# Kernel tuning notes

Measured on AMD Instinct MI355X. Metric: run time of the kernel, lower is better.

## Reference

```python
import jax, jax.numpy as jnp
import numpy as np

N_HEADS = 8
N_POINTS = 4
LN_EPS = 1e-5


def _ln(x, g, b):
    m = jnp.mean(x, -1, keepdims=True)
    v = jnp.mean((x - m) ** 2, -1, keepdims=True)
    return (x - m) * jax.lax.rsqrt(v + LN_EPS) * g + b


def _mha(q, k, v, wq, bq, wk, bk, wv, bv, wo, bo):
    B, Lq, C = q.shape
    Dh = C // N_HEADS
    Q = (q @ wq.T + bq).reshape(B, Lq, N_HEADS, Dh)
    K = (k @ wk.T + bk).reshape(B, -1, N_HEADS, Dh)
    V = (v @ wv.T + bv).reshape(B, -1, N_HEADS, Dh)
    s = jnp.einsum('bqhd,bkhd->bhqk', Q, K) * (1.0 / float(np.sqrt(Dh)))
    a = jax.nn.softmax(s, -1)
    o = jnp.einsum('bhqk,bkhd->bqhd', a, V).reshape(B, Lq, C)
    return o @ wo.T + bo


def _ref_points(h, w, L):
    ry = jnp.linspace(0.5, h - 0.5, h) / h
    rx = jnp.linspace(0.5, w - 0.5, w) / w
    gy, gx = jnp.meshgrid(ry, rx, indexing='ij')
    ref = jnp.stack([gx.reshape(-1), gy.reshape(-1)], -1)[None]  # (1, h*w, 2)
    return jnp.broadcast_to(ref[:, :, None, :], (1, h * w, L, 2))


def _deform_core(value, shapes, starts, loc, aw):
    # value: (B, Len_in, H, Dh); loc: (B, Lq, H, L, P, 2); aw: (B, Lq, H, L, P)
    B, _, H, Dh = value.shape
    Lq, P = loc.shape[1], loc.shape[4]
    out = jnp.zeros((B, H, Lq, Dh), value.dtype)
    for l in range(shapes.shape[0]):
        Hl, Wl = int(shapes[l, 0]), int(shapes[l, 1])
        s = int(starts[l])
        v = value[:, s:s + Hl * Wl].transpose(0, 2, 1, 3)  # (B, H, Hl*Wl, Dh)
        # grid_sample(align_corners=False, padding_mode='zeros') pixel coords
        xl = loc[:, :, :, l, :, 0] * Wl - 0.5  # (B, Lq, H, P)
        yl = loc[:, :, :, l, :, 1] * Hl - 0.5
        x0 = jnp.floor(xl); y0 = jnp.floor(yl)
        fx = xl - x0; fy = yl - y0
        x0 = x0.astype(jnp.int32); y0 = y0.astype(jnp.int32)
        acc = jnp.zeros((B, H, Lq, P, Dh), value.dtype)
        for dy, dx in ((0, 0), (0, 1), (1, 0), (1, 1)):
            xi = x0 + dx; yi = y0 + dy
            wgt = (fx if dx else 1.0 - fx) * (fy if dy else 1.0 - fy)
            valid = ((xi >= 0) & (xi < Wl) & (yi >= 0) & (yi < Hl)).astype(value.dtype)
            idx = (jnp.clip(yi, 0, Hl - 1) * Wl + jnp.clip(xi, 0, Wl - 1))
            idx = idx.transpose(0, 2, 1, 3).reshape(B, H, Lq * P)
            g = jnp.take_along_axis(v, idx[..., None], axis=2).reshape(B, H, Lq, P, Dh)
            acc = acc + g * (wgt * valid).transpose(0, 2, 1, 3)[..., None]
        out = out + jnp.einsum('bhqpd,bqhp->bhqd', acc, aw[:, :, :, l])
    return out.transpose(0, 2, 1, 3).reshape(B, Lq, H * Dh)


def reference(tgt, query_pos, src, wq, bq, wk, bk, wv, bv, wo, bo, ln2_g, ln2_b,
              w_off, b_off, w_attn, b_attn, w_val, b_val, w_cout, b_cout,
              ln1_g, ln1_b, w1, b1, w2, b2, ln3_g, ln3_b,
              src_spatial_shapes, level_start_index, h, w):
    shapes = np.asarray(src_spatial_shapes)
    starts = np.asarray(level_start_index)
    h = int(h); w = int(w)
    L = shapes.shape[0]
    B, Lq, C = tgt.shape
    Dh = C // N_HEADS
    # --- self attention (post-LN residual) ---
    q = tgt + query_pos
    t2 = _mha(q, q, tgt, wq, bq, wk, bk, wv, bv, wo, bo)
    t = _ln(tgt + t2, ln2_g, ln2_b)
    # --- MSDeformAttn cross attention ---
    qc = t + query_pos
    value = (src @ w_val.T + b_val).reshape(B, -1, N_HEADS, Dh)
    off = (qc @ w_off.T + b_off).reshape(B, Lq, N_HEADS, L, N_POINTS, 2)
    aw = (qc @ w_attn.T + b_attn).reshape(B, Lq, N_HEADS, L * N_POINTS)
    aw = jax.nn.softmax(aw, -1).reshape(B, Lq, N_HEADS, L, N_POINTS)
    norm = jnp.stack([shapes[:, 1].astype(np.float32), shapes[:, 0].astype(np.float32)], -1)  # (L,2): (W,H)
    rp = _ref_points(h, w, L)  # (1, Lq, L, 2)
    loc = rp[:, :, None, :, None, :] + off / norm[None, None, None, :, None, :]
    samp = _deform_core(value, shapes, starts, loc, aw)
    t2 = samp @ w_cout.T + b_cout
    t = _ln(t + t2, ln1_g, ln1_b)
    # --- FFN ---
    t2 = jax.nn.relu(t @ w1.T + b1) @ w2.T + b2
    t = _ln(t + t2, ln3_g, ln3_b)
    return t


def setup_inputs() -> dict:
    key = jax.random.key(0)
    B, C, L, P, dff = 2, 256, 4, 4, 1024
    h = w = 48
    shapes = np.array([[48, 48], [24, 24], [12, 12], [6, 6]], np.int32)
    starts = np.array([0, 2304, 2880, 3024], np.int32)
    Len_in = 3060
    Lq = h * w
    ks = iter(jax.random.split(key, 40))
    def rn(shape, s=0.02):
        return jax.random.normal(next(ks), shape, jnp.float32) * s
    return dict(
        tgt=rn((B, Lq, C), 1.0), query_pos=rn((B, Lq, C), 1.0), src=rn((B, Len_in, C), 1.0),
        wq=rn((C, C)), bq=rn((C,)), wk=rn((C, C)), bk=rn((C,)), wv=rn((C, C)), bv=rn((C,)),
        wo=rn((C, C)), bo=rn((C,)),
        ln2_g=jnp.ones((C,)), ln2_b=jnp.zeros((C,)),
        w_off=rn((N_HEADS * L * P * 2, C)), b_off=rn((N_HEADS * L * P * 2,)),
        w_attn=rn((N_HEADS * L * P, C)), b_attn=rn((N_HEADS * L * P,)),
        w_val=rn((C, C)), b_val=rn((C,)), w_cout=rn((C, C)), b_cout=rn((C,)),
        ln1_g=jnp.ones((C,)), ln1_b=jnp.zeros((C,)),
        w1=rn((dff, C)), b1=rn((dff,)), w2=rn((C, dff)), b2=rn((C,)),
        ln3_g=jnp.ones((C,)), ln3_b=jnp.zeros((C,)),
        src_spatial_shapes=shapes, level_start_index=starts, h=h, w=w)
```

## Files before the change

kernel.cpp:

```cpp
#include <hip/hip_runtime.h>
#include <hip/hip_bf16.h>
#include <math.h>

typedef __hip_bfloat16 bf16;
typedef __attribute__((ext_vector_type(8))) short short8;
typedef __attribute__((ext_vector_type(4))) short short4v;
typedef __attribute__((ext_vector_type(4))) float f32x4;

static constexpr int B   = 2;
static constexpr int LQ  = 2304;
static constexpr int C   = 256;
static constexpr int NH  = 8;
static constexpr int DH  = 32;
static constexpr int NL  = 4;
static constexpr int NP  = 4;
static constexpr int LEN = 3060;
static constexpr int DFF = 1024;
static constexpr int MQ  = B * LQ;
static constexpr int MV  = B * LEN;
static constexpr int SZ1 = MQ * C;

#define MFMA16(a, b, c) __builtin_amdgcn_mfma_f32_16x16x32_bf16(a, b, c, 0, 0, 0)

__device__ __forceinline__ float ldf(const void* p, size_t i, int bf) {
  return bf ? __bfloat162float(((const bf16*)p)[i]) : ((const float*)p)[i];
}
__device__ __forceinline__ short fl2s(float v) {
  bf16 h = __float2bfloat16(v);
  return *(short*)&h;
}
__device__ __forceinline__ short fl2s_fast(float v) {
  union { float f; unsigned u; } x; x.f = v;
  return (short)((x.u + 0x8000u) >> 16);
}
__device__ __forceinline__ float s2fl(short s) {
  return __bfloat162float(*(bf16*)&s);
}
__device__ __forceinline__ int wire_is_bf16(const unsigned* gprobe) {
  return gprobe[0] == 0x3F803F80u;
}
__device__ __forceinline__ float ldbias(const void* b, int n, int fl) {
  return fl ? s2fl(((const short*)b)[n]) : s2fl(fl2s(((const float*)b)[n]));
}
__device__ __forceinline__ short8 add2bf(short8 a, short8 b) {
  short8 r;
#pragma unroll
  for (int j = 0; j < 8; ++j) r[j] = fl2s(s2fl(a[j]) + s2fl(b[j]));
  return r;
}

struct GemmJob {
  int Xmode;
  const short* Xbf; const void* Xwire; const void* Xwire2;
  const void* Wwire; const void* bwire;
  void* Y;
  int M, N, K, ldY, col0, relu, out_mode, nblk_x;
  float qscale;
};
struct GemmBatch { GemmJob j[4]; int start[5]; int njobs; };

template <int MR>
__global__ __launch_bounds__(256) void gemm_mfma(GemmBatch nb,
                                                 const unsigned* __restrict__ gprobe) {
  constexpr int MT = MR / 64;
  const int fl = wire_is_bf16(gprobe);
  int id = blockIdx.x;
  int jj = 0;
  while (jj + 1 < nb.njobs && id >= nb.start[jj + 1]) ++jj;
  const GemmJob jb = nb.j[jj];
  const int local = id - nb.start[jj];
  const int bx = local % jb.nblk_x;
  const int by = local / jb.nblk_x;
  const int M = jb.M, N = jb.N, K = jb.K;

  __shared__ short Xs[MR][72];
  __shared__ short Ws[64][72];
  const int tid = threadIdx.x;
  const int wave = tid >> 6, lane = tid & 63;
  const int quad = lane >> 4, l16 = lane & 15;
  const int m0 = bx * MR, n0 = by * 64;
  f32x4 acc[MT][4];
#pragma unroll
  for (int mt = 0; mt < MT; ++mt)
#pragma unroll
    for (int nt = 0; nt < 4; ++nt) acc[mt][nt] = f32x4{0.f, 0.f, 0.f, 0.f};

  const int xrow = (MR == 128) ? (tid >> 1) : (tid >> 2);
  const int xcol = (MR == 128) ? ((tid & 1) * 32) : ((tid & 3) * 16);
  constexpr int XU = (MR == 128) ? 4 : 2;
  const int wrow = tid >> 2;
  const int wcol = (tid & 3) * 16;
  int xr = m0 + xrow; if (xr >= M) xr = M - 1;

  const short* xp16 = nullptr; const float* xpf = nullptr;
  const short* tp16 = nullptr; const short* pp16 = nullptr;
  const float* tpf  = nullptr; const float* ppf  = nullptr;
  if (jb.Xmode == 0) {
    xp16 = jb.Xbf + (size_t)xr * K;
  } else if (jb.Xmode == 2) {
    if (fl) xp16 = (const short*)jb.Xwire + (size_t)xr * K;
    else    xpf  = (const float*)jb.Xwire + (size_t)xr * K;
  } else {
    if (fl) { tp16 = (const short*)jb.Xwire + (size_t)xr * K;
              pp16 = (const short*)jb.Xwire2 + (size_t)xr * K; }
    else    { tpf  = (const float*)jb.Xwire + (size_t)xr * K;
              ppf  = (const float*)jb.Xwire2 + (size_t)xr * K; }
  }
  const short* wp16 = (const short*)jb.Wwire;
  const float* wpf  = (const float*)jb.Wwire;
  const size_t wro = (size_t)(n0 + wrow) * K;

  for (int k0 = 0; k0 < K; k0 += 64) {
    if (xp16) {
#pragma unroll
      for (int u = 0; u < XU; ++u)
        *(short8*)&Xs[xrow][xcol + u * 8] = *(const short8*)(xp16 + k0 + xcol + u * 8);
    } else if (xpf) {
#pragma unroll
      for (int u = 0; u < XU; ++u) {
        const float* s = xpf + k0 + xcol + u * 8;
        short8 r;
#pragma unroll
        for (int j = 0; j < 8; ++j) r[j] = fl2s(s[j]);
        *(short8*)&Xs[xrow][xcol + u * 8] = r;
      }
    } else if (tp16) {
#pragma unroll
      for (int u = 0; u < XU; ++u) {
        short8 t8 = *(const short8*)(tp16 + k0 + xcol + u * 8);
        short8 p8 = *(const short8*)(pp16 + k0 + xcol + u * 8);
        *(short8*)&Xs[xrow][xcol + u * 8] = add2bf(t8, p8);
      }
    } else {
#pragma unroll
      for (int u = 0; u < XU; ++u) {
        const float* t = tpf + k0 + xcol + u * 8;
        const float* p = ppf + k0 + xcol + u * 8;
        short8 r;
#pragma unroll
        for (int j = 0; j < 8; ++j) r[j] = fl2s(t[j] + p[j]);
        *(short8*)&Xs[xrow][xcol + u * 8] = r;
      }
    }
    if (fl) {
      const short* wp = wp16 + wro + k0 + wcol;
      *(short8*)&Ws[wrow][wcol]     = *(const short8*)(wp);
      *(short8*)&Ws[wrow][wcol + 8] = *(const short8*)(wp + 8);
    } else {
      const float* wp = wpf + wro + k0 + wcol;
      short8 w0, w1;
#pragma unroll
      for (int j = 0; j < 8; ++j) { w0[j] = fl2s(wp[j]); w1[j] = fl2s(wp[8 + j]); }
      *(short8*)&Ws[wrow][wcol]     = w0;
      *(short8*)&Ws[wrow][wcol + 8] = w1;
    }
    __syncthreads();
#pragma unroll
    for (int kc = 0; kc < 2; ++kc) {
#pragma unroll
      for (int mt = 0; mt < MT; ++mt) {
        short8 a = *(const short8*)&Xs[wave * (16 * MT) + mt * 16 + l16][kc * 32 + quad * 8];
#pragma unroll
        for (int nt = 0; nt < 4; ++nt) {
          short8 b = *(const short8*)&Ws[nt * 16 + l16][kc * 32 + quad * 8];
          acc[mt][nt] = MFMA16(a, b, acc[mt][nt]);
        }
      }
    }
    __syncthreads();
  }

  if (jb.out_mode == 2) {
#pragma unroll
    for (int mt = 0; mt < MT; ++mt) {
      const int mbase = m0 + wave * (16 * MT) + mt * 16 + quad * 4;
      const int b = mbase / LQ;
      const int qb_ = mbase - b * LQ;
#pragma unroll
      for (int nt = 0; nt < 4; ++nt) {
        const int n = n0 + nt * 16 + l16;
        const float bv = ldbias(jb.bwire, n, fl);
        short4v v4;
#pragma unroll
        for (int r = 0; r < 4; ++r) v4[r] = fl2s(acc[mt][nt][r] + bv);
        *(short4v*)((short*)jb.Y + (size_t)(b * 256 + n) * LQ + qb_) = v4;
      }
    }
    return;
  }
#pragma unroll
  for (int mt = 0; mt < MT; ++mt)
#pragma unroll
    for (int nt = 0; nt < 4; ++nt) {
      const int n = n0 + nt * 16 + l16;
      const float bv = ldbias(jb.bwire, n, fl);
#pragma unroll
      for (int r = 0; r < 4; ++r) {
        const int m = m0 + wave * (16 * MT) + mt * 16 + quad * 4 + r;
        if (m < M) {
          float v = (acc[mt][nt][r] + bv) * jb.qscale;
          if (jb.relu) v = fmaxf(v, 0.f);
          if (jb.out_mode == 1)
            ((short*)jb.Y)[(size_t)m * jb.ldY + jb.col0 + n] = fl2s(v);
          else
            ((float*)jb.Y)[(size_t)m * jb.ldY + jb.col0 + n] = v;
        }
      }
    }
}

__global__ __launch_bounds__(256) void ln_kern(const void* __restrict__ A, int a_mode,
                                               const float* __restrict__ R,
                                               const void* __restrict__ g,
                                               const void* __restrict__ be,
                                               float* __restrict__ Yf32,
                                               short* __restrict__ Y16,
                                               void* __restrict__ Yfinal,
                                               const void* __restrict__ pos,
                                               short* __restrict__ Yqc,
                                               int rows, const unsigned* __restrict__ gprobe) {
  const int fl = wire_is_bf16(gprobe);
  const int row = blockIdx.x * 4 + (threadIdx.x >> 6);
  const int lane = threadIdx.x & 63;
  if (row >= rows) return;
  const int c0 = lane * 4;
  const size_t base = (size_t)row * C + c0;

  float x[4];
  if (a_mode == 1 && fl) {
    short4v a4 = *(const short4v*)((const short*)A + base);
#pragma unroll
    for (int j = 0; j < 4; ++j) x[j] = s2fl(a4[j]);
  } else {
    f32x4 a4 = *(const f32x4*)((const float*)A + base);
#pragma unroll
    for (int j = 0; j < 4; ++j) x[j] = a4[j];
  }
  f32x4 r4 = *(const f32x4*)(R + base);
  float s = 0.f, s2 = 0.f;
#pragma unroll
  for (int j = 0; j < 4; ++j) { x[j] += r4[j]; s += x[j]; s2 += x[j] * x[j]; }
#pragma unroll
  for (int off = 32; off > 0; off >>= 1) {
    s += __shfl_xor(s, off);
    s2 += __shfl_xor(s2, off);
  }
  const float mean = s * (1.f / C);
  const float var = fmaxf(s2 * (1.f / C) - mean * mean, 0.f);
  const float inv = rsqrtf(var + 1e-5f);

  float gv[4], bvv[4];
  if (fl) {
    short4v g4 = *(const short4v*)((const short*)g + c0);
    short4v b4 = *(const short4v*)((const short*)be + c0);
#pragma unroll
    for (int j = 0; j < 4; ++j) { gv[j] = s2fl(g4[j]); bvv[j] = s2fl(b4[j]); }
  } else {
    f32x4 g4 = *(const f32x4*)((const float*)g + c0);
    f32x4 b4 = *(const f32x4*)((const float*)be + c0);
#pragma unroll
    for (int j = 0; j < 4; ++j) { gv[j] = g4[j]; bvv[j] = b4[j]; }
  }
  float y[4];
#pragma unroll
  for (int j = 0; j < 4; ++j) y[j] = (x[j] - mean) * inv * gv[j] + bvv[j];

  if (Yfinal) {
    if (fl) {
      short4v o;
#pragma unroll
      for (int j = 0; j < 4; ++j) o[j] = fl2s(y[j]);
      *(short4v*)((short*)Yfinal + base) = o;
    } else {
      f32x4 o;
#pragma unroll
      for (int j = 0; j < 4; ++j) o[j] = y[j];
      *(f32x4*)((float*)Yfinal + base) = o;
    }
    return;
  }
  if (Yf32) {
    f32x4 o;
#pragma unroll
    for (int j = 0; j < 4; ++j) o[j] = y[j];
    *(f32x4*)(Yf32 + base) = o;
  }
  if (Y16) {
    short4v o;
#pragma unroll
    for (int j = 0; j < 4; ++j) o[j] = fl2s(y[j]);
    *(short4v*)(Y16 + base) = o;
  }
  if (Yqc) {
    float pv[4];
    if (fl) {
      short4v p4 = *(const short4v*)((const short*)pos + base);
#pragma unroll
      for (int j = 0; j < 4; ++j) pv[j] = s2fl(p4[j]);
    } else {
      f32x4 p4 = *(const f32x4*)((const float*)pos + base);
#pragma unroll
      for (int j = 0; j < 4; ++j) pv[j] = p4[j];
    }
    short4v o;
#pragma unroll
    for (int j = 0; j < 4; ++j) o[j] = fl2s(y[j] + pv[j]);
    *(short4v*)(Yqc + base) = o;
  }
}

__global__ __launch_bounds__(256) void flash_attn(const short* __restrict__ QK,
                                                  const short* __restrict__ Vt,
                                                  short* __restrict__ Op) {
  constexpr int LDQK = 512;
  constexpr int NC = LQ / 64;
  constexpr int NQT = 3;
  const int qb = blockIdx.x;
  const int bh = blockIdx.y;
  const int b = bh >> 3, h = bh & 7;
  const int tid = threadIdx.x;
  const int wave = tid >> 6, lane = tid & 63;
  const int quad = lane >> 4, l16 = lane & 15;

  __shared__ short Ps[4][16][68];
  __shared__ float lsh[256];

  const int q0 = qb * 48;
  const size_t rowb = (size_t)(b * LQ);
  const short* kcol = QK + 256 + h * DH + quad * 8;
  const short* vt0 = Vt + (size_t)(b * 256 + h * 32 + l16) * LQ + quad * 8;
  const short* vt1 = Vt + (size_t)(b * 256 + h * 32 + 16 + l16) * LQ + quad * 8;

  short8 qfrag[NQT];
#pragma unroll
  for (int qt = 0; qt < NQT; ++qt)
    qfrag[qt] = *(const short8*)(QK + (rowb + q0 + qt * 16 + l16) * LDQK + h * DH + quad * 8);

  f32x4 o0[NQT], o1[NQT];
  float lrow[NQT];
#pragma unroll
  for (int qt = 0; qt < NQT; ++qt) {
    o0[qt] = f32x4{0.f, 0.f, 0.f, 0.f};
    o1[qt] = f32x4{0.f, 0.f, 0.f, 0.f};
    lrow[qt] = 0.f;
  }

  short8 kf[4], vf[4];
  {
    const int k0 = wave * 64;
#pragma unroll
    for (int kt = 0; kt < 4; ++kt)
      kf[kt] = *(const short8*)(kcol + (rowb + k0 + kt * 16 + l16) * LDQK);
    vf[0] = *(const short8*)(vt0 + k0);
    vf[1] = *(const short8*)(vt0 + k0 + 32);
    vf[2] = *(const short8*)(vt1 + k0);
    vf[3] = *(const short8*)(vt1 + k0 + 32);
  }

  for (int c = wave; c < NC; c += 4) {
    short8 kn[4], vn[4];
    if (c + 4 < NC) {
      const int k0n = (c + 4) * 64;
#pragma unroll
      for (int kt = 0; kt < 4; ++kt)
        kn[kt] = *(const short8*)(kcol + (rowb + k0n + kt * 16 + l16) * LDQK);
      vn[0] = *(const short8*)(vt0 + k0n);
      vn[1] = *(const short8*)(vt0 + k0n + 32);
      vn[2] = *(const short8*)(vt1 + k0n);
      vn[3] = *(const short8*)(vt1 + k0n + 32);
    }

#pragma unroll
    for (int qt = 0; qt < NQT; ++qt) {
      f32x4 s[4];
#pragma unroll
      for (int kt = 0; kt < 4; ++kt) {
        f32x4 z = {0.f, 0.f, 0.f, 0.f};
        s[kt] = MFMA16(kf[kt], qfrag[qt], z);
      }

      float ps = 0.f;
#pragma unroll
      for (int kt = 0; kt < 4; ++kt)
#pragma unroll
        for (int r = 0; r < 4; ++r) {
          float p = __expf(s[kt][r]);
          s[kt][r] = p;
          ps += p;
        }
      lrow[qt] += ps;

#pragma unroll
      for (int kt = 0; kt < 4; ++kt) {
        short4v pk;
#pragma unroll
        for (int r = 0; r < 4; ++r) pk[r] = fl2s_fast(s[kt][r]);
        *(short4v*)&Ps[wave][l16][kt * 16 + quad * 4] = pk;
      }

#pragma unroll
      for (int half = 0; half < 2; ++half) {
        short4v a0 = *(const short4v*)&Ps[wave][l16][half * 32 + quad * 8];
        short4v a1 = *(const short4v*)&Ps[wave][l16][half * 32 + quad * 8 + 4];
        short8 afrag;
#pragma unroll
        for (int j = 0; j < 4; ++j) { afrag[j] = a0[j]; afrag[4 + j] = a1[j]; }
        o0[qt] = MFMA16(afrag, vf[half], o0[qt]);
        o1[qt] = MFMA16(afrag, vf[2 + half], o1[qt]);
      }
    }

#pragma unroll
    for (int kt = 0; kt < 4; ++kt) { kf[kt] = kn[kt]; vf[kt] = vn[kt]; }
  }

  float* obuf = (float*)&Ps[0][0][0];
  for (int qt = 0; qt < NQT; ++qt) {
    __syncthreads();
    lsh[(wave * 4 + quad) * 16 + l16] = lrow[qt];
#pragma unroll
    for (int r = 0; r < 4; ++r) {
      const int q = quad * 4 + r;
      obuf[(wave * 16 + q) * 32 + l16] = o0[qt][r];
      obuf[(wave * 16 + q) * 32 + 16 + l16] = o1[qt][r];
    }
    __syncthreads();
#pragma unroll
    for (int e = tid; e < 512; e += 256) {
      const int q = e >> 5, d = e & 31;
      float lg = 0.f;
#pragma unroll
      for (int i = 0; i < 16; ++i) lg += lsh[i * 16 + q];
      float ov = 0.f;
#pragma unroll
      for (int w = 0; w < 4; ++w) ov += obuf[(w * 16 + q) * 32 + d];
      Op[(rowb + q0 + qt * 16 + q) * C + h * DH + d] = fl2s_fast(ov / lg);
    }
  }
}

__global__ __launch_bounds__(256) void deform_kern(const short* __restrict__ value,
                                                   const float* __restrict__ oa,
                                                   const int* __restrict__ shapes,
                                                   const int* __restrict__ starts,
                                                   const int* __restrict__ hp,
                                                   const int* __restrict__ wp,
                                                   short* __restrict__ samp) {
  const int bq = blockIdx.x * 4 + (threadIdx.x >> 6);
  const int b = bq / LQ, q = bq % LQ;
  const int lane = threadIdx.x & 63;
  const int h_ = lane >> 3;
  const int d0 = (lane & 7) * 4;

  const int w0 = *wp, h0 = *hp;
  const int qx = q % w0, qy = q / w0;
  const float refx = (qx + 0.5f) / (float)w0;
  const float refy = (qy + 0.5f) / (float)h0;

  const float* offp = oa + (size_t)bq * 384 + h_ * 32;
  const float* awraw = oa + (size_t)bq * 384 + 256 + h_ * 16;

  float e[16];
  float mm = -1e30f;
#pragma unroll
  for (int j = 0; j < 16; ++j) mm = fmaxf(mm, awraw[j]);
  float ssum = 0.f;
#pragma unroll
  for (int j = 0; j < 16; ++j) {
    e[j] = __expf(awraw[j] - mm);
    ssum += e[j];
  }
  const float sinv = 1.f / ssum;

  float acc0 = 0.f, acc1 = 0.f, acc2 = 0.f, acc3 = 0.f;
  for (int l = 0; l < NL; ++l) {
    const int Hl = shapes[l * 2 + 0];
    const int Wl = shapes[l * 2 + 1];
    const int st = starts[l];
    const short* vbase = value + ((size_t)(b * LEN + st)) * C + h_ * DH + d0;
#pragma unroll
    for (int p = 0; p < NP; ++p) {
      const float ox = offp[l * 8 + p * 2 + 0];
      const float oy = offp[l * 8 + p * 2 + 1];
      const float a = e[l * 4 + p] * sinv;
      const float xl = refx * Wl + ox - 0.5f;
      const float yl = refy * Hl + oy - 0.5f;
      const float x0f = floorf(xl), y0f = floorf(yl);
      const float fx = xl - x0f, fy = yl - y0f;
      const int x0 = (int)x0f, y0 = (int)y0f;
#pragma unroll
      for (int corner = 0; corner < 4; ++corner) {
        const int dx = corner & 1, dy = corner >> 1;
        const int xi = x0 + dx, yi = y0 + dy;
        const float wx = dx ? fx : 1.f - fx;
        const float wy = dy ? fy : 1.f - fy;
        const bool valid = (xi >= 0) & (xi < Wl) & (yi >= 0) & (yi < Hl);
        if (valid) {
          const float w = a * wx * wy;
          short4v v4 = *(const short4v*)(vbase + (size_t)(yi * Wl + xi) * C);
          acc0 += w * s2fl(v4[0]);
          acc1 += w * s2fl(v4[1]);
          acc2 += w * s2fl(v4[2]);
          acc3 += w * s2fl(v4[3]);
        }
      }
    }
  }
  short4v out;
  out[0] = fl2s(acc0); out[1] = fl2s(acc1); out[2] = fl2s(acc2); out[3] = fl2s(acc3);
  *(short4v*)(samp + (size_t)bq * C + h_ * DH + d0) = out;
}

extern "C" void kernel_launch(void* const* d_in, const int* in_sizes, int n_in,
                              void* d_out, int out_size, void* d_ws, size_t ws_size,
                              hipStream_t stream) {
  const void* tgt       = d_in[0];
  const void* query_pos = d_in[1];
  const void* src       = d_in[2];
  const void* wq = d_in[3];  const void* bq = d_in[4];
  const void* wk = d_in[5];  const void* bk = d_in[6];
  const void* wv = d_in[7];  const void* bv = d_in[8];
  const void* wo = d_in[9];  const void* bo = d_in[10];
  const void* ln2_g = d_in[11]; const void* ln2_b = d_in[12];
  const void* w_off = d_in[13]; const void* b_off = d_in[14];
  const void* w_attn = d_in[15]; const void* b_attn = d_in[16];
  const void* w_val = d_in[17]; const void* b_val = d_in[18];
  const void* w_cout = d_in[19]; const void* b_cout = d_in[20];
  const void* ln1_g = d_in[21]; const void* ln1_b = d_in[22];
  const void* w1 = d_in[23]; const void* b1 = d_in[24];
  const void* w2 = d_in[25]; const void* b2 = d_in[26];
  const void* ln3_g = d_in[27]; const void* ln3_b = d_in[28];
  const int* shapes = (const int*)d_in[29];
  const int* starts = (const int*)d_in[30];
  const int* hp = (const int*)d_in[31];
  const int* wp = (const int*)d_in[32];
  const unsigned* gprobe = (const unsigned*)ln2_g;

  short* q16    = (short*)((char*)d_ws + 256);
  short* qk_out = q16 + SZ1;
  short* vt16   = qk_out + (size_t)MQ * 512;
  short* ao16   = vt16 + SZ1;
  short* valb   = ao16 + SZ1;
  short* ffn1   = valb + (size_t)MV * C;
  short* t1_16  = ffn1 + (size_t)MQ * DFF;
  float* t2a    = (float*)(t1_16 + SZ1);
  float* t_32   = t2a + SZ1;
  float* t1_32  = t_32 + SZ1;
  float* oa     = t1_32 + SZ1;

  const float scale = 1.f / sqrtf((float)DH);
  const dim3 blk(256);
  const int NX128 = MQ / 128;
  const int NX64  = MQ / 64;
  const int NXV   = (MV + 127) / 128;

  {
    GemmBatch nb;
    nb.njobs = 4;
    nb.j[0] = {4, nullptr, tgt, query_pos, wq, bq, qk_out,
               MQ, 256, 256, 512, 0, 0, 1, NX128, scale};
    nb.j[1] = {4, nullptr, tgt, query_pos, wk, bk, qk_out,
               MQ, 256, 256, 512, 256, 0, 1, NX128, 1.f};
    nb.j[2] = {2, nullptr, tgt, nullptr, wv, bv, vt16,
               MQ, 256, 256, 0, 0, 0, 2, NX128, 1.f};
    nb.j[3] = {2, nullptr, src, nullptr, w_val, b_val, valb,
               MV, 256, 256, 256, 0, 0, 1, NXV, 1.f};
    nb.start[0] = 0;
    nb.start[1] = NX128 * 4;
    nb.start[2] = nb.start[1] + NX128 * 4;
    nb.start[3] = nb.start[2] + NX128 * 4;
    nb.start[4] = nb.start[3] + NXV * 4;
    gemm_mfma<128><<<nb.start[4], blk, 0, stream>>>(nb, gprobe);
  }
  flash_attn<<<dim3(LQ / 48, B * NH), blk, 0, stream>>>(qk_out, vt16, ao16);

  {
    GemmBatch nb;
    nb.njobs = 1;
    nb.j[0] = {0, ao16, nullptr, nullptr, wo, bo, t2a,
               MQ, 256, 256, 256, 0, 0, 0, NX64, 1.f};
    nb.start[0] = 0; nb.start[1] = NX64 * 4;
    gemm_mfma<64><<<nb.start[1], blk, 0, stream>>>(nb, gprobe);
  }
  ln_kern<<<MQ / 4, blk, 0, stream>>>(tgt, 1, t2a, ln2_g, ln2_b,
                                      t_32, nullptr, nullptr, query_pos, q16, MQ, gprobe);

  {
    GemmBatch nb;
    nb.njobs = 2;
    nb.j[0] = {0, q16, nullptr, nullptr, w_off, b_off, oa,
               MQ, 256, 256, 384, 0, 0, 0, NX64, 1.f};
    nb.j[1] = {0, q16, nullptr, nullptr, w_attn, b_attn, oa,
               MQ, 128, 256, 384, 256, 0, 0, NX64, 1.f};
    nb.start[0] = 0;
    nb.start[1] = NX64 * 4;
    nb.start[2] = nb.start[1] + NX64 * 2;
    gemm_mfma<64><<<nb.start[2], blk, 0, stream>>>(nb, gprobe);
  }
  deform_kern<<<MQ / 4, blk, 0, stream>>>(valb, oa, shapes, starts, hp, wp, ao16);

  {
    GemmBatch nb;
    nb.njobs = 1;
    nb.j[0] = {0, ao16, nullptr, nullptr, w_cout, b_cout, t2a,
               MQ, 256, 256, 256, 0, 0, 0, NX64, 1.f};
    nb.start[0] = 0; nb.start[1] = NX64 * 4;
    gemm_mfma<64><<<nb.start[1], blk, 0, stream>>>(nb, gprobe);
  }
  ln_kern<<<MQ / 4, blk, 0, stream>>>(t_32, 2, t2a, ln1_g, ln1_b,
                                      t1_32, t1_16, nullptr, nullptr, nullptr, MQ, gprobe);

  {
    GemmBatch nb;
    nb.njobs = 1;
    nb.j[0] = {0, t1_16, nullptr, nullptr, w1, b1, ffn1,
               MQ, 1024, 256, 1024, 0, 1, 1, NX128, 1.f};
    nb.start[0] = 0; nb.start[1] = NX128 * 16;
    gemm_mfma<128><<<nb.start[1], blk, 0, stream>>>(nb, gprobe);
  }
  {
    GemmBatch nb;
    nb.njobs = 1;
    nb.j[0] = {0, ffn1, nullptr, nullptr, w2, b2, t2a,
               MQ, 256, 1024, 256, 0, 0, 0, NX64, 1.f};
    nb.start[0] = 0; nb.start[1] = NX64 * 4;
    gemm_mfma<64><<<nb.start[1], blk, 0, stream>>>(nb, gprobe);
  }
  ln_kern<<<MQ / 4, blk, 0, stream>>>(t1_32, 2, t2a, ln3_g, ln3_b,
                                      nullptr, nullptr, d_out, nullptr, nullptr, MQ, gprobe);
}
```

Baseline: 284.6 us.

## Fuse N=256 GEMMs with residual LayerNorm via per-panel atomic completion counter

```diff
diff --git a/kernel.cpp b/kernel.cpp
--- a/kernel.cpp
+++ b/kernel.cpp
@@ -19,6 +19,7 @@
 static constexpr int MQ  = B * LQ;
 static constexpr int MV  = B * LEN;
 static constexpr int SZ1 = MQ * C;
+static constexpr int NPANEL = MQ / 64;
 
 #define MFMA16(a, b, c) __builtin_amdgcn_mfma_f32_16x16x32_bf16(a, b, c, 0, 0, 0)
 
@@ -57,13 +58,15 @@
   int M, N, K, ldY, col0, relu, out_mode, nblk_x;
   float qscale;
 };
-struct GemmBatch { GemmJob j[4]; int start[5]; int njobs; };
+struct GemmBatch { GemmJob j[4]; int start[5]; int njobs; int* cz; int czn; };
 
 template <int MR>
 __global__ __launch_bounds__(256) void gemm_mfma(GemmBatch nb,
                                                  const unsigned* __restrict__ gprobe) {
   constexpr int MT = MR / 64;
   const int fl = wire_is_bf16(gprobe);
+  const int tid = threadIdx.x;
+  if (nb.cz && blockIdx.x == 0 && tid < nb.czn) nb.cz[tid] = 0;
   int id = blockIdx.x;
   int jj = 0;
   while (jj + 1 < nb.njobs && id >= nb.start[jj + 1]) ++jj;
@@ -75,7 +78,6 @@
 
   __shared__ short Xs[MR][72];
   __shared__ short Ws[64][72];
-  const int tid = threadIdx.x;
   const int wave = tid >> 6, lane = tid & 63;
   const int quad = lane >> 4, l16 = lane & 15;
   const int m0 = bx * MR, n0 = by * 64;
@@ -209,103 +211,175 @@
     }
 }
 
-__global__ __launch_bounds__(256) void ln_kern(const void* __restrict__ A, int a_mode,
-                                               const float* __restrict__ R,
-                                               const void* __restrict__ g,
-                                               const void* __restrict__ be,
-                                               float* __restrict__ Yf32,
-                                               short* __restrict__ Y16,
-                                               void* __restrict__ Yfinal,
-                                               const void* __restrict__ pos,
-                                               short* __restrict__ Yqc,
-                                               int rows, const unsigned* __restrict__ gprobe) {
+struct G64Ln {
+  const short* X; const void* Wwire; const void* bwire; int K;
+  float* t2a;
+  const void* A; int a_mode;
+  const void* g; const void* be;
+  float* Yf32; short* Y16; void* Yfinal;
+  const void* pos; short* Yqc;
+  int* cnt;
+};
+
+__global__ __launch_bounds__(256) void gemm64_ln(G64Ln a,
+                                                 const unsigned* __restrict__ gprobe) {
   const int fl = wire_is_bf16(gprobe);
-  const int row = blockIdx.x * 4 + (threadIdx.x >> 6);
-  const int lane = threadIdx.x & 63;
-  if (row >= rows) return;
+  const int K = a.K;
+  const int bx = blockIdx.x % NPANEL;
+  const int by = blockIdx.x / NPANEL;
+
+  __shared__ short Xs[64][72];
+  __shared__ short Ws[64][72];
+  __shared__ int lastf;
+
+  const int tid = threadIdx.x;
+  const int wave = tid >> 6, lane = tid & 63;
+  const int quad = lane >> 4, l16 = lane & 15;
+  const int m0 = bx * 64, n0 = by * 64;
+
+  f32x4 acc[4];
+#pragma unroll
+  for (int nt = 0; nt < 4; ++nt) acc[nt] = f32x4{0.f, 0.f, 0.f, 0.f};
+
+  const int xrow = tid >> 2, xcol = (tid & 3) * 16;
+  const int wrow = tid >> 2, wcol = (tid & 3) * 16;
+  const short* xp = a.X + (size_t)(m0 + xrow) * K;
+  const short* wp16 = (const short*)a.Wwire;
+  const float* wpf  = (const float*)a.Wwire;
+  const size_t wro = (size_t)(n0 + wrow) * K;
+
+  for (int k0 = 0; k0 < K; k0 += 64) {
+#pragma unroll
+    for (int u = 0; u < 2; ++u)
+      *(short8*)&Xs[xrow][xcol + u * 8] = *(const short8*)(xp + k0 + xcol + u * 8);
+    if (fl) {
+      const short* wp = wp16 + wro + k0 + wcol;
+      *(short8*)&Ws[wrow][wcol]     = *(const short8*)(wp);
+      *(short8*)&Ws[wrow][wcol + 8] = *(const short8*)(wp + 8);
+    } else {
+      const float* wp = wpf + wro + k0 + wcol;
+      short8 w0, w1;
+#pragma unroll
+      for (int j = 0; j < 8; ++j) { w0[j] = fl2s(wp[j]); w1[j] = fl2s(wp[8 + j]); }
+      *(short8*)&Ws[wrow][wcol]     = w0;
+      *(short8*)&Ws[wrow][wcol + 8] = w1;
+    }
+    __syncthreads();
+#pragma unroll
+    for (int kc = 0; kc < 2; ++kc) {
+      short8 a8 = *(const short8*)&Xs[wave * 16 + l16][kc * 32 + quad * 8];
+#pragma unroll
+      for (int nt = 0; nt < 4; ++nt) {
+        short8 b8 = *(const short8*)&Ws[nt * 16 + l16][kc * 32 + quad * 8];
+        acc[nt] = MFMA16(a8, b8, acc[nt]);
+      }
+    }
+    __syncthreads();
+  }
+
+#pragma unroll
+  for (int nt = 0; nt < 4; ++nt) {
+    const int n = n0 + nt * 16 + l16;
+    const float bv = ldbias(a.bwire, n, fl);
+#pragma unroll
+    for (int r = 0; r < 4; ++r) {
+      const int m = m0 + wave * 16 + quad * 4 + r;
+      a.t2a[(size_t)m * C + n] = acc[nt][r] + bv;
+    }
+  }
+
+  __threadfence();
+  __syncthreads();
+  if (tid == 0) lastf = (atomicAdd(a.cnt + bx, 1) == 3);
+  __syncthreads();
+  if (!lastf) return;
+  __threadfence();
+
   const int c0 = lane * 4;
-  const size_t base = (size_t)row * C + c0;
-
-  float x[4];
-  if (a_mode == 1 && fl) {
-    short4v a4 = *(const short4v*)((const short*)A + base);
-#pragma unroll
-    for (int j = 0; j < 4; ++j) x[j] = s2fl(a4[j]);
-  } else {
-    f32x4 a4 = *(const f32x4*)((const float*)A + base);
-#pragma unroll
-    for (int j = 0; j < 4; ++j) x[j] = a4[j];
-  }
-  f32x4 r4 = *(const f32x4*)(R + base);
-  float s = 0.f, s2 = 0.f;
-#pragma unroll
-  for (int j = 0; j < 4; ++j) { x[j] += r4[j]; s += x[j]; s2 += x[j] * x[j]; }
-#pragma unroll
-  for (int off = 32; off > 0; off >>= 1) {
-    s += __shfl_xor(s, off);
-    s2 += __shfl_xor(s2, off);
-  }
-  const float mean = s * (1.f / C);
-  const float var = fmaxf(s2 * (1.f / C) - mean * mean, 0.f);
-  const float inv = rsqrtf(var + 1e-5f);
-
   float gv[4], bvv[4];
   if (fl) {
-    short4v g4 = *(const short4v*)((const short*)g + c0);
-    short4v b4 = *(const short4v*)((const short*)be + c0);
+    short4v g4 = *(const short4v*)((const short*)a.g + c0);
+    short4v b4 = *(const short4v*)((const short*)a.be + c0);
 #pragma unroll
     for (int j = 0; j < 4; ++j) { gv[j] = s2fl(g4[j]); bvv[j] = s2fl(b4[j]); }
   } else {
-    f32x4 g4 = *(const f32x4*)((const float*)g + c0);
-    f32x4 b4 = *(const f32x4*)((const float*)be + c0);
+    f32x4 g4 = *(const f32x4*)((const float*)a.g + c0);
+    f32x4 b4 = *(const f32x4*)((const float*)a.be + c0);
 #pragma unroll
     for (int j = 0; j < 4; ++j) { gv[j] = g4[j]; bvv[j] = b4[j]; }
   }
-  float y[4];
-#pragma unroll
-  for (int j = 0; j < 4; ++j) y[j] = (x[j] - mean) * inv * gv[j] + bvv[j];
-
-  if (Yfinal) {
-    if (fl) {
+
+  for (int rr = 0; rr < 16; ++rr) {
+    const int row = m0 + wave * 16 + rr;
+    const size_t base = (size_t)row * C + c0;
+    float x[4];
+    if (a.a_mode == 1 && fl) {
+      short4v a4 = *(const short4v*)((const short*)a.A + base);
+#pragma unroll
+      for (int j = 0; j < 4; ++j) x[j] = s2fl(a4[j]);
+    } else {
+      f32x4 a4 = *(const f32x4*)((const float*)a.A + base);
+#pragma unroll
+      for (int j = 0; j < 4; ++j) x[j] = a4[j];
+    }
+    f32x4 r4 = *(const f32x4*)(a.t2a + base);
+    float s = 0.f, s2 = 0.f;
+#pragma unroll
+    for (int j = 0; j < 4; ++j) { x[j] += r4[j]; s += x[j]; s2 += x[j] * x[j]; }
+#pragma unroll
+    for (int off = 32; off > 0; off >>= 1) {
+      s += __shfl_xor(s, off);
+      s2 += __shfl_xor(s2, off);
+    }
+    const float mean = s * (1.f / C);
+    const float var = fmaxf(s2 * (1.f / C) - mean * mean, 0.f);
+    const float inv = rsqrtf(var + 1e-5f);
+    float y[4];
+#pragma unroll
+    for (int j = 0; j < 4; ++j) y[j] = (x[j] - mean) * inv * gv[j] + bvv[j];
+
+    if (a.Yfinal) {
+      if (fl) {
+        short4v o;
+#pragma unroll
+        for (int j = 0; j < 4; ++j) o[j] = fl2s(y[j]);
+        *(short4v*)((short*)a.Yfinal + base) = o;
+      } else {
+        f32x4 o;
+#pragma unroll
+        for (int j = 0; j < 4; ++j) o[j] = y[j];
+        *(f32x4*)((float*)a.Yfinal + base) = o;
+      }
+      continue;
+    }
+    if (a.Yf32) {
+      f32x4 o;
+#pragma unroll
+      for (int j = 0; j < 4; ++j) o[j] = y[j];
+      *(f32x4*)(a.Yf32 + base) = o;
+    }
+    if (a.Y16) {
       short4v o;
 #pragma unroll
       for (int j = 0; j < 4; ++j) o[j] = fl2s(y[j]);
-      *(short4v*)((short*)Yfinal + base) = o;
-    } else {
-      f32x4 o;
-#pragma unroll
-      for (int j = 0; j < 4; ++j) o[j] = y[j];
-      *(f32x4*)((float*)Yfinal + base) = o;
-    }
-    return;
-  }
-  if (Yf32) {
-    f32x4 o;
-#pragma unroll
-    for (int j = 0; j < 4; ++j) o[j] = y[j];
-    *(f32x4*)(Yf32 + base) = o;
-  }
-  if (Y16) {
-    short4v o;
-#pragma unroll
-    for (int j = 0; j < 4; ++j) o[j] = fl2s(y[j]);
-    *(short4v*)(Y16 + base) = o;
-  }
-  if (Yqc) {
-    float pv[4];
-    if (fl) {
-      short4v p4 = *(const short4v*)((const short*)pos + base);
-#pragma unroll
-      for (int j = 0; j < 4; ++j) pv[j] = s2fl(p4[j]);
-    } else {
-      f32x4 p4 = *(const f32x4*)((const float*)pos + base);
-#pragma unroll
-      for (int j = 0; j < 4; ++j) pv[j] = p4[j];
-    }
-    short4v o;
-#pragma unroll
-    for (int j = 0; j < 4; ++j) o[j] = fl2s(y[j] + pv[j]);
-    *(short4v*)(Yqc + base) = o;
+      *(short4v*)(a.Y16 + base) = o;
+    }
+    if (a.Yqc) {
+      float pv[4];
+      if (fl) {
+        short4v p4 = *(const short4v*)((const short*)a.pos + base);
+#pragma unroll
+        for (int j = 0; j < 4; ++j) pv[j] = s2fl(p4[j]);
+      } else {
+        f32x4 p4 = *(const f32x4*)((const float*)a.pos + base);
+#pragma unroll
+        for (int j = 0; j < 4; ++j) pv[j] = p4[j];
+      }
+      short4v o;
+#pragma unroll
+      for (int j = 0; j < 4; ++j) o[j] = fl2s(y[j] + pv[j]);
+      *(short4v*)(a.Yqc + base) = o;
+    }
   }
 }
 
@@ -536,7 +610,10 @@
   const int* wp = (const int*)d_in[32];
   const unsigned* gprobe = (const unsigned*)ln2_g;
 
-  short* q16    = (short*)((char*)d_ws + 256);
+  int*   cnt0   = (int*)d_ws;
+  int*   cnt1   = cnt0 + NPANEL;
+  int*   cnt2   = cnt1 + NPANEL;
+  short* q16    = (short*)((char*)d_ws + 1024);
   short* qk_out = q16 + SZ1;
   short* vt16   = qk_out + (size_t)MQ * 512;
   short* ao16   = vt16 + SZ1;
@@ -557,6 +634,7 @@
   {
     GemmBatch nb;
     nb.njobs = 4;
+    nb.cz = cnt0; nb.czn = 3 * NPANEL;
     nb.j[0] = {4, nullptr, tgt, query_pos, wq, bq, qk_out,
                MQ, 256, 256, 512, 0, 0, 1, NX128, scale};
     nb.j[1] = {4, nullptr, tgt, query_pos, wk, bk, qk_out,
@@ -575,19 +653,19 @@
   flash_attn<<<dim3(LQ / 48, B * NH), blk, 0, stream>>>(qk_out, vt16, ao16);
 
   {
-    GemmBatch nb;
-    nb.njobs = 1;
-    nb.j[0] = {0, ao16, nullptr, nullptr, wo, bo, t2a,
-               MQ, 256, 256, 256, 0, 0, 0, NX64, 1.f};
-    nb.start[0] = 0; nb.start[1] = NX64 * 4;
-    gemm_mfma<64><<<nb.start[1], blk, 0, stream>>>(nb, gprobe);
-  }
-  ln_kern<<<MQ / 4, blk, 0, stream>>>(tgt, 1, t2a, ln2_g, ln2_b,
-                                      t_32, nullptr, nullptr, query_pos, q16, MQ, gprobe);
+    G64Ln a;
+    a.X = ao16; a.Wwire = wo; a.bwire = bo; a.K = 256; a.t2a = t2a;
+    a.A = tgt; a.a_mode = 1; a.g = ln2_g; a.be = ln2_b;
+    a.Yf32 = t_32; a.Y16 = nullptr; a.Yfinal = nullptr;
+    a.pos = query_pos; a.Yqc = q16;
+    a.cnt = cnt0;
+    gemm64_ln<<<NX64 * 4, blk, 0, stream>>>(a, gprobe);
+  }
 
   {
     GemmBatch nb;
     nb.njobs = 2;
+    nb.cz = nullptr; nb.czn = 0;
     nb.j[0] = {0, q16, nullptr, nullptr, w_off, b_off, oa,
                MQ, 256, 256, 384, 0, 0, 0, NX64, 1.f};
     nb.j[1] = {0, q16, nullptr, nullptr, w_attn, b_attn, oa,
@@ -600,32 +678,31 @@
   deform_kern<<<MQ / 4, blk, 0, stream>>>(valb, oa, shapes, starts, hp, wp, ao16);
 
   {
-    GemmBatch nb;
-    nb.njobs = 1;
-    nb.j[0] = {0, ao16, nullptr, nullptr, w_cout, b_cout, t2a,
-               MQ, 256, 256, 256, 0, 0, 0, NX64, 1.f};
-    nb.start[0] = 0; nb.start[1] = NX64 * 4;
-    gemm_mfma<64><<<nb.start[1], blk, 0, stream>>>(nb, gprobe);
-  }
-  ln_kern<<<MQ / 4, blk, 0, stream>>>(t_32, 2, t2a, ln1_g, ln1_b,
-                                      t1_32, t1_16, nullptr, nullptr, nullptr, MQ, gprobe);
+    G64Ln a;
+    a.X = ao16; a.Wwire = w_cout; a.bwire = b_cout; a.K = 256; a.t2a = t2a;
+    a.A = t_32; a.a_mode = 2; a.g = ln1_g; a.be = ln1_b;
+    a.Yf32 = t1_32; a.Y16 = t1_16; a.Yfinal = nullptr;
+    a.pos = nullptr; a.Yqc = nullptr;
+    a.cnt = cnt1;
+    gemm64_ln<<<NX64 * 4, blk, 0, stream>>>(a, gprobe);
+  }
 
   {
     GemmBatch nb;
     nb.njobs = 1;
+    nb.cz = nullptr; nb.czn = 0;
     nb.j[0] = {0, t1_16, nullptr, nullptr, w1, b1, ffn1,
                MQ, 1024, 256, 1024, 0, 1, 1, NX128, 1.f};
     nb.start[0] = 0; nb.start[1] = NX128 * 16;
     gemm_mfma<128><<<nb.start[1], blk, 0, stream>>>(nb, gprobe);
   }
   {
-    GemmBatch nb;
-    nb.njobs = 1;
-    nb.j[0] = {0, ffn1, nullptr, nullptr, w2, b2, t2a,
-               MQ, 256, 1024, 256, 0, 0, 0, NX64, 1.f};
-    nb.start[0] = 0; nb.start[1] = NX64 * 4;
-    gemm_mfma<64><<<nb.start[1], blk, 0, stream>>>(nb, gprobe);
-  }
-  ln_kern<<<MQ / 4, blk, 0, stream>>>(t1_32, 2, t2a, ln3_g, ln3_b,
-                                      nullptr, nullptr, d_out, nullptr, nullptr, MQ, gprobe);
-}
+    G64Ln a;
+    a.X = ffn1; a.Wwire = w2; a.bwire = b2; a.K = 1024; a.t2a = t2a;
+    a.A = t1_32; a.a_mode = 2; a.g = ln3_g; a.be = ln3_b;
+    a.Yf32 = nullptr; a.Y16 = nullptr; a.Yfinal = d_out;
+    a.pos = nullptr; a.Yqc = nullptr;
+    a.cnt = cnt2;
+    gemm64_ln<<<NX64 * 4, blk, 0, stream>>>(a, gprobe);
+  }
+}
```

New measurement: 405.2 us. +42.4%, slower.
